# Performance work log

Hardware: AMD Instinct MI355X
Metric: run time of the kernel (lower is better)

Reference implementation:

```python
import jax, jax.numpy as jnp
import numpy as np

D_IN = 1024
D_OUT = 1024
NUM_HEADS = 16
HEAD_DIM = D_OUT // NUM_HEADS


def setup_inputs() -> dict:
    key = jax.random.key(0)
    k_x, k_q, k_k, k_v, k_o, k_ob = jax.random.split(key, 6)
    s_in = 1.0 / np.sqrt(D_IN)
    s_out = 1.0 / np.sqrt(D_OUT)
    return {
        "x": jax.random.normal(k_x, (2, 2048, D_IN), dtype=jnp.float32),
        "W_q": jax.random.uniform(k_q, (D_IN, D_OUT), minval=-s_in, maxval=s_in, dtype=jnp.float32),
        "W_k": jax.random.uniform(k_k, (D_IN, D_OUT), minval=-s_in, maxval=s_in, dtype=jnp.float32),
        "W_v": jax.random.uniform(k_v, (D_IN, D_OUT), minval=-s_in, maxval=s_in, dtype=jnp.float32),
        "W_out": jax.random.uniform(k_o, (D_OUT, D_OUT), minval=-s_out, maxval=s_out, dtype=jnp.float32),
        "b_out": jax.random.uniform(k_ob, (D_OUT,), minval=-s_out, maxval=s_out, dtype=jnp.float32),
    }


def reference(x, W_q, W_k, W_v, W_out, b_out):
    b, t, _ = x.shape
    # projections (qkv_bias=False)
    q = (x @ W_q).reshape(b, t, NUM_HEADS, HEAD_DIM).transpose(0, 2, 1, 3)  # [b,h,t,d]
    k = (x @ W_k).reshape(b, t, NUM_HEADS, HEAD_DIM).transpose(0, 2, 1, 3)
    v = (x @ W_v).reshape(b, t, NUM_HEADS, HEAD_DIM).transpose(0, 2, 1, 3)
    scale = 1.0 / np.sqrt(HEAD_DIM).astype(np.float32)
    scores = jnp.einsum("bhqd,bhkd->bhqk", q, k) * scale  # [b,h,t,t]
    causal = jnp.triu(jnp.ones((t, t), dtype=bool), k=1)
    scores = jnp.where(causal, -jnp.inf, scores)
    weights = jax.nn.softmax(scores, axis=-1)
    # dropout p=0.0 -> identity
    context = jnp.einsum("bhqk,bhkd->bhqd", weights, v)
    context = context.transpose(0, 2, 1, 3).reshape(b, t, D_OUT)
    return context @ W_out + b_out
```

## Files before the change

kernel.cpp:

```cpp
#include <hip/hip_runtime.h>
#include <hip/hip_bf16.h>

#define B_  2
#define T_  2048
#define D_  1024
#define H_  16
#define DH_ 64
#define M_  (B_*T_)

typedef _Float16 f16;
typedef __attribute__((ext_vector_type(4))) _Float16 f16x4;
typedef __attribute__((ext_vector_type(8))) _Float16 f16x8;
typedef __attribute__((ext_vector_type(4))) float f32x4;

#define GLOAD_LDS(gp, lp) __builtin_amdgcn_global_load_lds( \
    (const __attribute__((address_space(1))) void*)(gp),    \
    (__attribute__((address_space(3))) void*)(lp), 16, 0, 0)

__global__ void prep(const float* __restrict__ x,
                     const float* __restrict__ wq, const float* __restrict__ wk,
                     const float* __restrict__ wv, const float* __restrict__ wo,
                     f16* __restrict__ xb, f16* __restrict__ wqkvT, f16* __restrict__ woutT) {
  __shared__ float tile[32][33];
  const int bid = blockIdx.x;
  if (bid < 2048) {
    size_t i = ((size_t)bid * 256 + threadIdx.x) * 8;
    float4 a = *(const float4*)(x + i);
    float4 b = *(const float4*)(x + i + 4);
    f16x8 o;
    o[0]=(f16)a.x; o[1]=(f16)a.y; o[2]=(f16)a.z; o[3]=(f16)a.w;
    o[4]=(f16)b.x; o[5]=(f16)b.y; o[6]=(f16)b.z; o[7]=(f16)b.w;
    *(f16x8*)(xb + i) = o;
  } else {
    const int b2 = bid - 2048;
    const int j = b2 >> 10, rem = b2 & 1023;
    const float* src = (j==0)?wq:(j==1)?wk:(j==2)?wv:wo;
    f16* dst = (j<3) ? (wqkvT + (size_t)j*D_*D_) : woutT;
    const int n0 = (rem & 31)*32, k0 = (rem >> 5)*32;
    const int tx = threadIdx.x & 31, ty = threadIdx.x >> 5;
    #pragma unroll
    for (int i=0;i<32;i+=8)
      tile[ty+i][tx] = src[(size_t)(k0+ty+i)*D_ + n0+tx];
    __syncthreads();
    #pragma unroll
    for (int i=0;i<32;i+=8)
      dst[(size_t)(n0+ty+i)*D_ + k0+tx] = (f16)tile[tx][ty+i];
  }
}

__launch_bounds__(256, 2)
__global__ void qkv_gemm(const f16* __restrict__ xb, const f16* __restrict__ wT,
                         f16* __restrict__ Qp, f16* __restrict__ Kp, f16* __restrict__ Vtp) {
  const int fid = blockIdx.x;
  const int g = fid & 7, r = fid >> 3;
  const int m0 = ((((r & 3) << 3) | g)) * 128;
  const int n0 = ((r >> 2) & 7) * 128;
  const int j  = r >> 5;
  const f16* B0 = wT + (size_t)j * D_ * D_;
  __shared__ alignas(16) char smem[65536];
  f16* AsF = (f16*)smem;
  f16* BsF = AsF + 2*128*64;
  const int tid = threadIdx.x;
  const int lane = tid & 63, wave = tid >> 6;
  const int ln = lane & 15, quad = lane >> 4;
  const int wm = wave >> 1, wn = wave & 1;

  f32x4 acc[4][4];
  #pragma unroll
  for (int a=0;a<4;++a)
    #pragma unroll
    for (int b=0;b<4;++b) acc[a][b] = f32x4{0.f,0.f,0.f,0.f};

  const bool swapped = (j < 2);
  const int slot_row[4] = { (0*256+tid)>>3, (1*256+tid)>>3, (2*256+tid)>>3, (3*256+tid)>>3 };

  #pragma unroll
  for (int p = 0; p < 4; ++p) {
    int slot = p*256 + tid;
    int row  = slot_row[p];
    int c    = (slot & 7) ^ (row & 7);
    GLOAD_LDS(xb + (size_t)(m0+row)*D_ + c*8, AsF + (size_t)slot*8);
    GLOAD_LDS(B0 + (size_t)(n0+row)*D_ + c*8, BsF + (size_t)slot*8);
  }
  __syncthreads();

  for (int it = 0; it < 16; ++it) {
    const f16* Ac = AsF + (it & 1)*8192;
    const f16* Bc = BsF + (it & 1)*8192;
    if (it < 15) {
      const int k1 = (it + 1) * 64;
      f16* An = AsF + ((it + 1) & 1)*8192;
      f16* Bn = BsF + ((it + 1) & 1)*8192;
      #pragma unroll
      for (int p = 0; p < 4; ++p) {
        int slot = p*256 + tid;
        int row  = slot_row[p];
        int c    = (slot & 7) ^ (row & 7);
        GLOAD_LDS(xb + (size_t)(m0+row)*D_ + k1 + c*8, An + (size_t)slot*8);
        GLOAD_LDS(B0 + (size_t)(n0+row)*D_ + k1 + c*8, Bn + (size_t)slot*8);
      }
    }
    #pragma unroll
    for (int ks = 0; ks < 2; ++ks) {
      const int cb = ((ks*4 + quad) ^ (ln & 7)) * 8;
      f16x8 af[4], bf[4];
      #pragma unroll
      for (int mt = 0; mt < 4; ++mt)
        af[mt] = *(const f16x8*)(Ac + (size_t)(wm*64 + mt*16 + ln)*64 + cb);
      #pragma unroll
      for (int nt = 0; nt < 4; ++nt)
        bf[nt] = *(const f16x8*)(Bc + (size_t)(wn*64 + nt*16 + ln)*64 + cb);
      if (swapped) {
        #pragma unroll
        for (int nt = 0; nt < 4; ++nt)
          #pragma unroll
          for (int mt = 0; mt < 4; ++mt)
            acc[nt][mt] = __builtin_amdgcn_mfma_f32_16x16x32_f16(bf[nt], af[mt], acc[nt][mt], 0, 0, 0);
      } else {
        #pragma unroll
        for (int mt = 0; mt < 4; ++mt)
          #pragma unroll
          for (int nt = 0; nt < 4; ++nt)
            acc[mt][nt] = __builtin_amdgcn_mfma_f32_16x16x32_f16(af[mt], bf[nt], acc[mt][nt], 0, 0, 0);
      }
    }
    __syncthreads();
  }

  if (swapped) {
    const float scale = (j == 0) ? 0.125f : 1.0f;
    f16* dstB = (j == 0) ? Qp : Kp;
    #pragma unroll
    for (int nt = 0; nt < 4; ++nt)
      #pragma unroll
      for (int mt = 0; mt < 4; ++mt) {
        int gm = m0 + wm*64 + mt*16 + ln;
        int gn = n0 + wn*64 + nt*16 + quad*4;
        int bb = gm >> 11, t = gm & (T_-1);
        int h  = gn >> 6,  dd = gn & (DH_-1);
        f16x4 v;
        #pragma unroll
        for (int rr = 0; rr < 4; ++rr) v[rr] = (f16)(acc[nt][mt][rr] * scale);
        *(f16x4*)&dstB[((((size_t)bb*H_ + h)*T_ + t)*DH_) + dd] = v;
      }
  } else {
    f16* VtS = (f16*)smem;
    #pragma unroll
    for (int mt = 0; mt < 4; ++mt)
      #pragma unroll
      for (int nt = 0; nt < 4; ++nt) {
        f16x4 v;
        v[0]=(f16)acc[mt][nt][0]; v[1]=(f16)acc[mt][nt][1];
        v[2]=(f16)acc[mt][nt][2]; v[3]=(f16)acc[mt][nt][3];
        *(f16x4*)&VtS[(size_t)(wn*64 + nt*16 + ln)*136 + wm*64 + mt*16 + quad*4] = v;
      }
    __syncthreads();
    int dd_loc = tid >> 1, half = tid & 1;
    int gn = n0 + dd_loc, h = gn >> 6, dd = gn & (DH_-1);
    int bb = m0 >> 11, tb = (m0 & (T_-1)) + half*64;
    f16* dst = Vtp + ((size_t)(bb*H_ + h)*DH_ + dd)*T_ + tb;
    const f16* src = VtS + (size_t)dd_loc*136 + half*64;
    #pragma unroll
    for (int u = 0; u < 8; ++u)
      *(uint4*)(dst + u*8) = *(const uint4*)(src + u*8);
  }
}

__launch_bounds__(256, 3)
__global__ void flash(const f16* __restrict__ Qp, const f16* __restrict__ Kp,
                      const f16* __restrict__ Vtp, f16* __restrict__ ctx) {
  const int fid = blockIdx.x;
  const int bh = fid & 31;
  const int qt = 31 - (fid >> 5);
  const int b = bh >> 4, h = bh & (H_-1);
  const f16* Kh = Kp  + (size_t)bh * T_ * DH_;
  const f16* Vh = Vtp + (size_t)bh * DH_ * T_;
  const f16* Qh = Qp  + (size_t)bh * T_ * DH_;
  const int tid = threadIdx.x, lane = tid & 63, w = tid >> 6;
  const int ln = lane & 15, quad = lane >> 4;
  __shared__ alignas(16) f16 Ks[2*64*64];
  __shared__ alignas(16) f16 Vs[2*64*64];
  __shared__ alignas(16) f16 Ps[64][72];

  const int qw = qt*64 + w*16;

  f16x8 qf[2];
  #pragma unroll
  for (int ks = 0; ks < 2; ++ks)
    qf[ks] = *(const f16x8*)&Qh[(size_t)(qw + ln)*DH_ + ks*32 + quad*8];

  f32x4 o[4];
  #pragma unroll
  for (int dt = 0; dt < 4; ++dt) o[dt] = f32x4{0.f,0.f,0.f,0.f};
  float l_part = 0.f;

  #pragma unroll
  for (int i = 0; i < 2; ++i) {
    int row = w*16 + i*8 + (lane >> 3);
    int c   = (lane & 7) ^ (row & 7);
    GLOAD_LDS(Kh + (size_t)row*DH_ + c*8, Ks + (w*128 + i*64 + lane)*8);
    GLOAD_LDS(Vh + (size_t)row*T_  + c*8, Vs + (w*128 + i*64 + lane)*8);
  }
  __syncthreads();

  for (int it = 0; it <= qt; ++it) {
    const f16* Kc = Ks + (it & 1)*4096;
    const f16* Vc = Vs + (it & 1)*4096;
    if (it < qt) {
      const int kv1 = (it + 1)*64;
      f16* Kn = Ks + ((it + 1) & 1)*4096;
      f16* Vn = Vs + ((it + 1) & 1)*4096;
      #pragma unroll
      for (int i = 0; i < 2; ++i) {
        int row = w*16 + i*8 + (lane >> 3);
        int c   = (lane & 7) ^ (row & 7);
        GLOAD_LDS(Kh + (size_t)(kv1 + row)*DH_ + c*8, Kn + (w*128 + i*64 + lane)*8);
        GLOAD_LDS(Vh + (size_t)row*T_ + kv1 + c*8,    Vn + (w*128 + i*64 + lane)*8);
      }
    }

    f32x4 s[4];
    #pragma unroll
    for (int kt = 0; kt < 4; ++kt) s[kt] = f32x4{0.f,0.f,0.f,0.f};
    #pragma unroll
    for (int ks = 0; ks < 2; ++ks) {
      f16x8 kx[4];
      #pragma unroll
      for (int kt = 0; kt < 4; ++kt)
        kx[kt] = *(const f16x8*)(Kc + (size_t)(kt*16 + ln)*64 + (((ks*4 + quad) ^ (ln & 7))*8));
      #pragma unroll
      for (int kt = 0; kt < 4; ++kt)
        s[kt] = __builtin_amdgcn_mfma_f32_16x16x32_f16(kx[kt], qf[ks], s[kt], 0, 0, 0);
    }
    if (it == qt) {
      const int kv0 = it*64;
      #pragma unroll
      for (int kt = 0; kt < 4; ++kt)
        #pragma unroll
        for (int rr = 0; rr < 4; ++rr)
          if (kv0 + kt*16 + quad*4 + rr > qw + ln) s[kt][rr] = -INFINITY;
    }
    #pragma unroll
    for (int kt = 0; kt < 4; ++kt) {
      f16x4 pk;
      #pragma unroll
      for (int rr = 0; rr < 4; ++rr) {
        float pe = __expf(s[kt][rr]);
        l_part += pe;
        pk[rr] = (f16)pe;
      }
      *(f16x4*)&Ps[w*16 + ln][kt*16 + quad*4] = pk;
    }
    asm volatile("" ::: "memory");

    #pragma unroll
    for (int ks = 0; ks < 2; ++ks) {
      f16x8 px = *(const f16x8*)&Ps[w*16 + ln][ks*32 + quad*8];
      #pragma unroll
      for (int dt = 0; dt < 4; ++dt) {
        f16x8 vy = *(const f16x8*)(Vc + (size_t)(dt*16 + ln)*64 + (((ks*4 + quad) ^ (ln & 7))*8));
        o[dt] = __builtin_amdgcn_mfma_f32_16x16x32_f16(px, vy, o[dt], 0, 0, 0);
      }
    }
    __syncthreads();
  }

  float l = l_part;
  l += __shfl_xor(l, 16, 64);
  l += __shfl_xor(l, 32, 64);
  float inv = 1.0f / l;
  #pragma unroll
  for (int rr = 0; rr < 4; ++rr) {
    float linv = __shfl(inv, quad*4 + rr, 64);
    int t = qt*64 + w*16 + quad*4 + rr;
    #pragma unroll
    for (int dt = 0; dt < 4; ++dt)
      ctx[(size_t)(b*T_ + t)*D_ + h*DH_ + dt*16 + ln] = (f16)(o[dt][rr] * linv);
  }
}

__launch_bounds__(256, 2)
__global__ void out_gemm(const f16* __restrict__ ctx, const f16* __restrict__ woT,
                         const float* __restrict__ bo, float* __restrict__ out) {
  const int fid = blockIdx.x;
  const int g = fid & 7, r = fid >> 3;
  const int m0 = ((((r & 3) << 3) | g)) * 128;
  const int n0 = (r >> 2) * 128;
  __shared__ alignas(16) f16 smem[4*128*64];
  f16* AsF = smem;
  f16* BsF = AsF + 2*128*64;
  const int tid = threadIdx.x;
  const int lane = tid & 63, wave = tid >> 6;
  const int ln = lane & 15, quad = lane >> 4;
  const int wm = wave >> 1, wn = wave & 1;

  f32x4 acc[4][4];
  #pragma unroll
  for (int a=0;a<4;++a)
    #pragma unroll
    for (int b=0;b<4;++b) acc[a][b] = f32x4{0.f,0.f,0.f,0.f};

  #pragma unroll
  for (int p = 0; p < 4; ++p) {
    int slot = p*256 + tid;
    int row  = slot >> 3;
    int c    = (slot & 7) ^ (row & 7);
    GLOAD_LDS(ctx + (size_t)(m0+row)*D_ + c*8, AsF + (size_t)slot*8);
    GLOAD_LDS(woT + (size_t)(n0+row)*D_ + c*8, BsF + (size_t)slot*8);
  }
  __syncthreads();

  for (int it = 0; it < 16; ++it) {
    const f16* Ac = AsF + (it & 1)*8192;
    const f16* Bc = BsF + (it & 1)*8192;
    if (it < 15) {
      const int k1 = (it + 1) * 64;
      f16* An = AsF + ((it + 1) & 1)*8192;
      f16* Bn = BsF + ((it + 1) & 1)*8192;
      #pragma unroll
      for (int p = 0; p < 4; ++p) {
        int slot = p*256 + tid;
        int row  = slot >> 3;
        int c    = (slot & 7) ^ (row & 7);
        GLOAD_LDS(ctx + (size_t)(m0+row)*D_ + k1 + c*8, An + (size_t)slot*8);
        GLOAD_LDS(woT + (size_t)(n0+row)*D_ + k1 + c*8, Bn + (size_t)slot*8);
      }
    }
    #pragma unroll
    for (int ks = 0; ks < 2; ++ks) {
      const int cb = ((ks*4 + quad) ^ (ln & 7)) * 8;
      f16x8 af[4], bf[4];
      #pragma unroll
      for (int mt = 0; mt < 4; ++mt)
        af[mt] = *(const f16x8*)(Ac + (size_t)(wm*64 + mt*16 + ln)*64 + cb);
      #pragma unroll
      for (int nt = 0; nt < 4; ++nt)
        bf[nt] = *(const f16x8*)(Bc + (size_t)(wn*64 + nt*16 + ln)*64 + cb);
      #pragma unroll
      for (int nt = 0; nt < 4; ++nt)
        #pragma unroll
        for (int mt = 0; mt < 4; ++mt)
          acc[nt][mt] = __builtin_amdgcn_mfma_f32_16x16x32_f16(bf[nt], af[mt], acc[nt][mt], 0, 0, 0);
    }
    __syncthreads();
  }

  #pragma unroll
  for (int nt = 0; nt < 4; ++nt) {
    int gn = n0 + wn*64 + nt*16 + quad*4;
    float4 bv = *(const float4*)&bo[gn];
    #pragma unroll
    for (int mt = 0; mt < 4; ++mt) {
      int gm = m0 + wm*64 + mt*16 + ln;
      float4 v;
      v.x = acc[nt][mt][0] + bv.x;
      v.y = acc[nt][mt][1] + bv.y;
      v.z = acc[nt][mt][2] + bv.z;
      v.w = acc[nt][mt][3] + bv.w;
      *(float4*)&out[(size_t)gm*D_ + gn] = v;
    }
  }
}

extern "C" void kernel_launch(void* const* d_in, const int* in_sizes, int n_in,
                              void* d_out, int out_size, void* d_ws, size_t ws_size,
                              hipStream_t stream) {
  const float* x  = (const float*)d_in[0];
  const float* wq = (const float*)d_in[1];
  const float* wk = (const float*)d_in[2];
  const float* wv = (const float*)d_in[3];
  const float* wo = (const float*)d_in[4];
  const float* bo = (const float*)d_in[5];
  float* out = (float*)d_out;

  f16* ws    = (f16*)d_ws;
  f16* xb    = ws;
  f16* wqkvT = xb    + (size_t)M_*D_;
  f16* woutT = wqkvT + (size_t)3*D_*D_;
  f16* Qb    = woutT + (size_t)D_*D_;
  f16* Kb    = Qb    + (size_t)M_*D_;
  f16* Vb    = Kb    + (size_t)M_*D_;
  f16* ctx   = Vb    + (size_t)M_*D_;

  prep<<<6144, 256, 0, stream>>>(x, wq, wk, wv, wo, xb, wqkvT, woutT);
  qkv_gemm<<<768, 256, 0, stream>>>(xb, wqkvT, Qb, Kb, Vb);
  flash<<<1024, 256, 0, stream>>>(Qb, Kb, Vb, ctx);
  out_gemm<<<256, 256, 0, stream>>>(ctx, woutT, bo, out);
}
```

Measured before the change: 162.6 us.

## Double flash query tile to 128 rows per block and interleave causal tile order

The flash kernel now processes 128 query rows per block, with each wave handling 32 rows as two 16-row groups. Each K/V tile loaded to shared memory is therefore reused across twice as many queries, and the grid is halved. Query tiles are interleaved long/short so blocks with heavy and light causal work alternate in the schedule, and waves skip fully masked KV tiles. The trade-offs are more registers per thread against the 3-blocks-per-CU launch bound, and fewer blocks to spread across CUs.

```diff
diff --git a/kernel.cpp b/kernel.cpp
--- a/kernel.cpp
+++ b/kernel.cpp
@@ -171,7 +171,8 @@
                       const f16* __restrict__ Vtp, f16* __restrict__ ctx) {
   const int fid = blockIdx.x;
   const int bh = fid & 31;
-  const int qt = 31 - (fid >> 5);
+  const int gg = fid >> 5;
+  const int qt = (gg & 1) ? (gg >> 1) : (15 - (gg >> 1));
   const int b = bh >> 4, h = bh & (H_-1);
   const f16* Kh = Kp  + (size_t)bh * T_ * DH_;
   const f16* Vh = Vtp + (size_t)bh * DH_ * T_;
@@ -180,102 +181,121 @@
   const int ln = lane & 15, quad = lane >> 4;
   __shared__ alignas(16) f16 Ks[2*64*64];
   __shared__ alignas(16) f16 Vs[2*64*64];
-  __shared__ alignas(16) f16 Ps[64][72];
-
-  const int qw = qt*64 + w*16;
-
-  f16x8 qf[2];
-  #pragma unroll
-  for (int ks = 0; ks < 2; ++ks)
-    qf[ks] = *(const f16x8*)&Qh[(size_t)(qw + ln)*DH_ + ks*32 + quad*8];
-
-  f32x4 o[4];
-  #pragma unroll
-  for (int dt = 0; dt < 4; ++dt) o[dt] = f32x4{0.f,0.f,0.f,0.f};
-  float l_part = 0.f;
-
-  #pragma unroll
-  for (int i = 0; i < 2; ++i) {
-    int row = w*16 + i*8 + (lane >> 3);
-    int c   = (lane & 7) ^ (row & 7);
-    GLOAD_LDS(Kh + (size_t)row*DH_ + c*8, Ks + (w*128 + i*64 + lane)*8);
-    GLOAD_LDS(Vh + (size_t)row*T_  + c*8, Vs + (w*128 + i*64 + lane)*8);
-  }
+  __shared__ alignas(16) f16 Ps[128][72];
+
+  const int qw = qt*128 + w*32;
+
+  f16x8 qf[2][2];
+  #pragma unroll
+  for (int qg = 0; qg < 2; ++qg)
+    #pragma unroll
+    for (int ks = 0; ks < 2; ++ks)
+      qf[qg][ks] = *(const f16x8*)&Qh[(size_t)(qw + qg*16 + ln)*DH_ + ks*32 + quad*8];
+
+  f32x4 o[2][4];
+  #pragma unroll
+  for (int qg = 0; qg < 2; ++qg)
+    #pragma unroll
+    for (int dt = 0; dt < 4; ++dt) o[qg][dt] = f32x4{0.f,0.f,0.f,0.f};
+  float l_part[2] = {0.f, 0.f};
+
+  const int srow0 = (0*256 + tid) >> 3, sc0 = ((0*256 + tid) & 7) ^ (srow0 & 7);
+  const int srow1 = (1*256 + tid) >> 3, sc1 = ((1*256 + tid) & 7) ^ (srow1 & 7);
+  GLOAD_LDS(Kh + (size_t)srow0*DH_ + sc0*8, Ks + (size_t)(0*256+tid)*8);
+  GLOAD_LDS(Kh + (size_t)srow1*DH_ + sc1*8, Ks + (size_t)(1*256+tid)*8);
+  GLOAD_LDS(Vh + (size_t)srow0*T_  + sc0*8, Vs + (size_t)(0*256+tid)*8);
+  GLOAD_LDS(Vh + (size_t)srow1*T_  + sc1*8, Vs + (size_t)(1*256+tid)*8);
   __syncthreads();
 
-  for (int it = 0; it <= qt; ++it) {
+  const int nkv = 2*qt + 2;
+  for (int it = 0; it < nkv; ++it) {
+    const int kv0 = it * 64;
     const f16* Kc = Ks + (it & 1)*4096;
     const f16* Vc = Vs + (it & 1)*4096;
-    if (it < qt) {
-      const int kv1 = (it + 1)*64;
+    if (it + 1 < nkv) {
+      const int kv1 = kv0 + 64;
       f16* Kn = Ks + ((it + 1) & 1)*4096;
       f16* Vn = Vs + ((it + 1) & 1)*4096;
-      #pragma unroll
-      for (int i = 0; i < 2; ++i) {
-        int row = w*16 + i*8 + (lane >> 3);
-        int c   = (lane & 7) ^ (row & 7);
-        GLOAD_LDS(Kh + (size_t)(kv1 + row)*DH_ + c*8, Kn + (w*128 + i*64 + lane)*8);
-        GLOAD_LDS(Vh + (size_t)row*T_ + kv1 + c*8,    Vn + (w*128 + i*64 + lane)*8);
-      }
-    }
-
-    f32x4 s[4];
-    #pragma unroll
-    for (int kt = 0; kt < 4; ++kt) s[kt] = f32x4{0.f,0.f,0.f,0.f};
-    #pragma unroll
-    for (int ks = 0; ks < 2; ++ks) {
-      f16x8 kx[4];
-      #pragma unroll
-      for (int kt = 0; kt < 4; ++kt)
-        kx[kt] = *(const f16x8*)(Kc + (size_t)(kt*16 + ln)*64 + (((ks*4 + quad) ^ (ln & 7))*8));
-      #pragma unroll
-      for (int kt = 0; kt < 4; ++kt)
-        s[kt] = __builtin_amdgcn_mfma_f32_16x16x32_f16(kx[kt], qf[ks], s[kt], 0, 0, 0);
-    }
-    if (it == qt) {
-      const int kv0 = it*64;
-      #pragma unroll
-      for (int kt = 0; kt < 4; ++kt)
-        #pragma unroll
-        for (int rr = 0; rr < 4; ++rr)
-          if (kv0 + kt*16 + quad*4 + rr > qw + ln) s[kt][rr] = -INFINITY;
-    }
-    #pragma unroll
-    for (int kt = 0; kt < 4; ++kt) {
-      f16x4 pk;
-      #pragma unroll
-      for (int rr = 0; rr < 4; ++rr) {
-        float pe = __expf(s[kt][rr]);
-        l_part += pe;
-        pk[rr] = (f16)pe;
-      }
-      *(f16x4*)&Ps[w*16 + ln][kt*16 + quad*4] = pk;
-    }
-    asm volatile("" ::: "memory");
-
-    #pragma unroll
-    for (int ks = 0; ks < 2; ++ks) {
-      f16x8 px = *(const f16x8*)&Ps[w*16 + ln][ks*32 + quad*8];
-      #pragma unroll
-      for (int dt = 0; dt < 4; ++dt) {
-        f16x8 vy = *(const f16x8*)(Vc + (size_t)(dt*16 + ln)*64 + (((ks*4 + quad) ^ (ln & 7))*8));
-        o[dt] = __builtin_amdgcn_mfma_f32_16x16x32_f16(px, vy, o[dt], 0, 0, 0);
+      GLOAD_LDS(Kh + (size_t)(kv1 + srow0)*DH_ + sc0*8, Kn + (size_t)(0*256+tid)*8);
+      GLOAD_LDS(Kh + (size_t)(kv1 + srow1)*DH_ + sc1*8, Kn + (size_t)(1*256+tid)*8);
+      GLOAD_LDS(Vh + (size_t)srow0*T_ + kv1 + sc0*8,    Vn + (size_t)(0*256+tid)*8);
+      GLOAD_LDS(Vh + (size_t)srow1*T_ + kv1 + sc1*8,    Vn + (size_t)(1*256+tid)*8);
+    }
+
+    if (kv0 <= qw + 31) {
+      f32x4 s[2][4];
+      #pragma unroll
+      for (int qg = 0; qg < 2; ++qg)
+        #pragma unroll
+        for (int kt = 0; kt < 4; ++kt) s[qg][kt] = f32x4{0.f,0.f,0.f,0.f};
+      #pragma unroll
+      for (int ks = 0; ks < 2; ++ks) {
+        f16x8 kx[4];
+        #pragma unroll
+        for (int kt = 0; kt < 4; ++kt)
+          kx[kt] = *(const f16x8*)(Kc + (size_t)(kt*16 + ln)*64 + (((ks*4 + quad) ^ (ln & 7))*8));
+        #pragma unroll
+        for (int qg = 0; qg < 2; ++qg)
+          #pragma unroll
+          for (int kt = 0; kt < 4; ++kt)
+            s[qg][kt] = __builtin_amdgcn_mfma_f32_16x16x32_f16(kx[kt], qf[qg][ks], s[qg][kt], 0, 0, 0);
+      }
+      if (kv0 + 63 > qw) {
+        #pragma unroll
+        for (int qg = 0; qg < 2; ++qg)
+          #pragma unroll
+          for (int kt = 0; kt < 4; ++kt)
+            #pragma unroll
+            for (int rr = 0; rr < 4; ++rr)
+              if (kv0 + kt*16 + quad*4 + rr > qw + qg*16 + ln) s[qg][kt][rr] = -INFINITY;
+      }
+      #pragma unroll
+      for (int qg = 0; qg < 2; ++qg)
+        #pragma unroll
+        for (int kt = 0; kt < 4; ++kt) {
+          f16x4 pk;
+          #pragma unroll
+          for (int rr = 0; rr < 4; ++rr) {
+            float pe = __expf(s[qg][kt][rr]);
+            l_part[qg] += pe;
+            pk[rr] = (f16)pe;
+          }
+          *(f16x4*)&Ps[w*32 + qg*16 + ln][kt*16 + quad*4] = pk;
+        }
+      asm volatile("" ::: "memory");
+
+      #pragma unroll
+      for (int ks = 0; ks < 2; ++ks) {
+        f16x8 vy[4];
+        #pragma unroll
+        for (int dt = 0; dt < 4; ++dt)
+          vy[dt] = *(const f16x8*)(Vc + (size_t)(dt*16 + ln)*64 + (((ks*4 + quad) ^ (ln & 7))*8));
+        #pragma unroll
+        for (int qg = 0; qg < 2; ++qg) {
+          f16x8 px = *(const f16x8*)&Ps[w*32 + qg*16 + ln][ks*32 + quad*8];
+          #pragma unroll
+          for (int dt = 0; dt < 4; ++dt)
+            o[qg][dt] = __builtin_amdgcn_mfma_f32_16x16x32_f16(px, vy[dt], o[qg][dt], 0, 0, 0);
+        }
       }
     }
     __syncthreads();
   }
 
-  float l = l_part;
-  l += __shfl_xor(l, 16, 64);
-  l += __shfl_xor(l, 32, 64);
-  float inv = 1.0f / l;
-  #pragma unroll
-  for (int rr = 0; rr < 4; ++rr) {
-    float linv = __shfl(inv, quad*4 + rr, 64);
-    int t = qt*64 + w*16 + quad*4 + rr;
-    #pragma unroll
-    for (int dt = 0; dt < 4; ++dt)
-      ctx[(size_t)(b*T_ + t)*D_ + h*DH_ + dt*16 + ln] = (f16)(o[dt][rr] * linv);
+  #pragma unroll
+  for (int qg = 0; qg < 2; ++qg) {
+    float l = l_part[qg];
+    l += __shfl_xor(l, 16, 64);
+    l += __shfl_xor(l, 32, 64);
+    float inv = 1.0f / l;
+    #pragma unroll
+    for (int rr = 0; rr < 4; ++rr) {
+      float linv = __shfl(inv, quad*4 + rr, 64);
+      int t = qw + qg*16 + quad*4 + rr;
+      #pragma unroll
+      for (int dt = 0; dt < 4; ++dt)
+        ctx[(size_t)(b*T_ + t)*D_ + h*DH_ + dt*16 + ln] = (f16)(o[qg][dt][rr] * linv);
+    }
   }
 }
 
@@ -384,6 +404,6 @@
 
   prep<<<6144, 256, 0, stream>>>(x, wq, wk, wv, wo, xb, wqkvT, woutT);
   qkv_gemm<<<768, 256, 0, stream>>>(xb, wqkvT, Qb, Kb, Vb);
-  flash<<<1024, 256, 0, stream>>>(Qb, Kb, Vb, ctx);
+  flash<<<512, 256, 0, stream>>>(Qb, Kb, Vb, ctx);
   out_gemm<<<256, 256, 0, stream>>>(ctx, woutT, bo, out);
 }
```

After: 176.5 us. 1.09x slower.
